# Performance work log

Hardware: AMD Instinct MI355X
Metric: run time of the kernel (lower is better)

Reference implementation:

```python
import jax, jax.numpy as jnp
import numpy as np

N, D, MAX_DEG, B = 100000, 256, 128, 1024
FANOUTS = (25, 10)
OUT = 128  # per-branch output dim; concat doubles it


def setup_inputs() -> dict:
    key = jax.random.key(0)
    ks = jax.random.split(key, 8)
    s1 = 1.0 / np.sqrt(D)
    return {
        "ids": jax.random.randint(ks[0], (B,), 0, N),
        "adj": jax.random.randint(ks[1], (N, MAX_DEG), 0, N),
        "feats": jax.random.normal(ks[2], (N, D), dtype=jnp.float32),
        "W1x": jax.random.normal(ks[3], (OUT, D), dtype=jnp.float32) * s1,
        "b1x": jnp.zeros((OUT,), jnp.float32),
        "W1n": jax.random.normal(ks[4], (OUT, D), dtype=jnp.float32) * s1,
        "b1n": jnp.zeros((OUT,), jnp.float32),
        "W2x": jax.random.normal(ks[5], (OUT, 2 * OUT), dtype=jnp.float32) * s1,
        "b2x": jnp.zeros((OUT,), jnp.float32),
        "W2n": jax.random.normal(ks[6], (OUT, 2 * OUT), dtype=jnp.float32) * s1,
        "b2n": jnp.zeros((OUT,), jnp.float32),
    }


def _sample(adj, ids, n_samples, key):
    # uniform_neib_sampler: one shared random column permutation, take first n
    perm = jax.random.permutation(key, adj.shape[1])
    return adj[ids][:, perm[:n_samples]].reshape(-1)  # flattened neighbor ids


def _agg(x, neibs, Wx, bx, Wn, bn, act):
    # MeanAggregator: concat(fc_x(x), fc_neib(mean over neighbors))
    m = neibs.reshape(x.shape[0], -1, neibs.shape[-1]).mean(axis=1)
    out = jnp.concatenate([x @ Wx.T + bx, m @ Wn.T + bn], axis=-1)
    return act(out) if act is not None else out


def reference(ids, adj, feats, W1x, b1x, W1n, b1n, W2x, b2x, W2n, b2n):
    k1, k2 = jax.random.split(jax.random.key(42))
    ids1 = _sample(adj, ids, FANOUTS[0], k1)      # [B*25]
    ids2 = _sample(adj, ids1, FANOUTS[1], k2)     # [B*25*10]
    h = [feats[ids], feats[ids1], feats[ids2]]    # gathers: the memory-bound core
    # layer 1 (relu) applied to each consecutive (self, neighbor) pair
    h = [_agg(h[k], h[k + 1], W1x, b1x, W1n, b1n, jax.nn.relu) for k in range(2)]
    # layer 2 (no activation)
    h = [_agg(h[0], h[1], W2x, b2x, W2n, b2n, None)]
    return h[0]  # [B, 256]
```

## Files before the change

kernel.cpp:

```cpp
#include <hip/hip_runtime.h>
#include <stdint.h>
#include <stddef.h>
#include <algorithm>


#define D       256
#define D4      64
#define BATCH   1024
#define F1      25
#define F2      10
#define MAXDEG  128
#define OUTD    128
#define SP      264
#define ZP      260

struct Perms { int p1[F1]; int p2[F2]; };

static inline uint32_t rotl32(uint32_t x, int d){ return (x<<d)|(x>>(32-d)); }

static void tf2x32(uint32_t k0, uint32_t k1, uint32_t x0, uint32_t x1,
                   uint32_t* o0, uint32_t* o1){
  uint32_t ks0=k0, ks1=k1, ks2 = k0^k1^0x1BD11BDAu;
  static const int rot[2][4] = {{13,15,26,6},{17,29,16,24}};
  x0 += ks0; x1 += ks1;
  for (int g=0; g<5; ++g){
    const int* r = rot[g&1];
    for (int i=0;i<4;++i){ x0 += x1; x1 = rotl32(x1, r[i]) ^ x0; }
    switch(g){
      case 0: x0 += ks1; x1 += ks2 + 1u; break;
      case 1: x0 += ks2; x1 += ks0 + 2u; break;
      case 2: x0 += ks0; x1 += ks1 + 3u; break;
      case 3: x0 += ks1; x1 += ks2 + 4u; break;
      default:x0 += ks2; x1 += ks0 + 5u; break;
    }
  }
  *o0 = x0; *o1 = x1;
}

static void mkperm(uint32_t ka, uint32_t kb, int n, int* outp){
  uint32_t ska, skb;
  tf2x32(ka, kb, 0u, 1u, &ska, &skb);
  uint32_t bits[MAXDEG];
  int idxs[MAXDEG];
  for (int i=0;i<MAXDEG;++i){
    uint32_t y0,y1; tf2x32(ska,skb, 0u,(uint32_t)i, &y0,&y1);
    bits[i] = y0 ^ y1;
    idxs[i] = i;
  }
  std::stable_sort(idxs, idxs+MAXDEG,
                   [&](int a,int b){ return bits[a] < bits[b]; });
  for (int j=0;j<n;++j) outp[j] = idxs[j];
}

static void compute_perms(Perms& P){
  uint32_t k1a,k1b,k2a,k2b;
  tf2x32(0u,42u, 0u,0u, &k1a,&k1b);
  tf2x32(0u,42u, 0u,1u, &k2a,&k2b);
  mkperm(k1a,k1b, F1, P.p1);
  mkperm(k2a,k2b, F2, P.p2);
}

typedef short s16x8 __attribute__((ext_vector_type(8)));
typedef float f32x4 __attribute__((ext_vector_type(4)));

__device__ __forceinline__ uint16_t f2bf(float f){
  uint32_t u = __float_as_uint(f);
  u += 0x7fffu + ((u >> 16) & 1u);
  return (uint16_t)(u >> 16);
}
__device__ __forceinline__ float bf2f(uint16_t h){
  return __uint_as_float(((uint32_t)h) << 16);
}

__global__ __launch_bounds__(256) void pack_k(
    const float* __restrict__ W1x, const float* __restrict__ W1n,
    const float* __restrict__ W2x, const float* __restrict__ W2n,
    uint16_t* __restrict__ WB, float* __restrict__ W2T){
  int g = blockIdx.x*256 + threadIdx.x;
  if (g < 8192){
    int kt = g >> 10, ct = (g >> 6) & 15, lane = g & 63;
    int n = ct*16 + (lane & 15);
    int k = kt*32 + (lane >> 4)*8;
    const float* src = (n < OUTD) ? (W1x + (size_t)n*D + k)
                                  : (W1n + (size_t)(n-OUTD)*D + k);
    float4 f0 = *(const float4*)src;
    float4 f1 = *(const float4*)(src + 4);
    uint32_t p[4] = {
      (uint32_t)f2bf(f0.x) | ((uint32_t)f2bf(f0.y)<<16),
      (uint32_t)f2bf(f0.z) | ((uint32_t)f2bf(f0.w)<<16),
      (uint32_t)f2bf(f1.x) | ((uint32_t)f2bf(f1.y)<<16),
      (uint32_t)f2bf(f1.z) | ((uint32_t)f2bf(f1.w)<<16) };
    *(uint4*)(WB + (size_t)g*8) = *(uint4*)p;
  } else {
    int idx = g - 8192;
    int k = idx >> 8, o = idx & 255;
    W2T[idx] = (o < OUTD) ? W2x[(size_t)o*D + k]
                          : W2n[(size_t)(o-OUTD)*D + k];
  }
}

__global__ __launch_bounds__(256, 4) void mega6_k(
    const float4* __restrict__ feats4,
    const int* __restrict__ ids, const int* __restrict__ adj,
    const uint16_t* __restrict__ WB, const float* __restrict__ W2T,
    const float* __restrict__ b1x, const float* __restrict__ b1n,
    const float* __restrict__ b2x, const float* __restrict__ b2n,
    float* __restrict__ out, Perms P)
{
  __shared__ uint16_t S[64*SP];
  __shared__ float    M2s[D];
  __shared__ float    Z0s[D];
  __shared__ int      sids[26];
  __shared__ int      nidx[F1*F2];

  const int b    = blockIdx.x;
  const int tid  = threadIdx.x;
  const int lane = tid & 63;
  const int w    = tid >> 6;
  const int ln   = lane & 15;
  const int q    = lane >> 4;
  const int id   = ids[b];
  uint16_t* Z = S;

  if (tid < F1) sids[tid] = adj[(size_t)id*MAXDEG + P.p1[tid]];
  if (tid == F1) sids[F1] = id;
  __syncthreads();
  if (tid < F1*F2){
    int j = tid / F2, u = tid - (tid/F2)*F2;
    nidx[tid] = adj[(size_t)sids[j]*MAXDEG + P.p2[u]];
  }
  __syncthreads();

  float4 va[7];
  #pragma unroll
  for (int l=0;l<7;++l){
    int idx = tid + l*256;
    if (idx < 26*D4)
      va[l] = feats4[(size_t)sids[idx>>6]*D4 + (idx&63)];
  }
  #pragma unroll 2
  for (int t=0;t<7;++t){
    int j = w + 4*t;
    if (j < F1){
      const int* np = &nidx[j*F2];
      float4 s = {0.f,0.f,0.f,0.f};
      #pragma unroll
      for (int u=0;u<F2;++u){
        float4 v = feats4[(size_t)np[u]*D4 + lane];
        s.x+=v.x; s.y+=v.y; s.z+=v.z; s.w+=v.w;
      }
      const float inv = 1.f/F2;
      uint32_t p[2] = {
        (uint32_t)f2bf(s.x*inv) | ((uint32_t)f2bf(s.y*inv)<<16),
        (uint32_t)f2bf(s.z*inv) | ((uint32_t)f2bf(s.w*inv)<<16) };
      *(uint2*)(S + (26+j)*SP + lane*4) = *(uint2*)p;
    }
  }
  #pragma unroll
  for (int l=0;l<7;++l){
    int idx = tid + l*256;
    if (idx < 26*D4){
      int r = idx>>6, c4 = idx&63;
      uint32_t p[2] = { (uint32_t)f2bf(va[l].x) | ((uint32_t)f2bf(va[l].y)<<16),
                        (uint32_t)f2bf(va[l].z) | ((uint32_t)f2bf(va[l].w)<<16) };
      *(uint2*)(S + r*SP + c4*4) = *(uint2*)p;
    }
  }
  __syncthreads();

  {
    float s = 0.f;
    #pragma unroll
    for (int r=0;r<F1;++r) s += bf2f(S[r*SP + tid]);
    S[51*SP + tid] = f2bf(s * (1.f/F1));
  }
  __syncthreads();

  f32x4 acc[4][4];
  #pragma unroll
  for (int mt=0;mt<4;++mt)
    #pragma unroll
    for (int nt=0;nt<4;++nt) acc[mt][nt] = (f32x4){0.f,0.f,0.f,0.f};

  #pragma unroll 2
  for (int kt = 0; kt < 8; ++kt){
    s16x8 af[4], bf[4];
    #pragma unroll
    for (int mt=0;mt<4;++mt)
      af[mt] = *(const s16x8*)(S + (mt*16 + ln)*SP + kt*32 + q*8);
    #pragma unroll
    for (int nt=0;nt<4;++nt)
      bf[nt] = *(const s16x8*)(WB + (size_t)((kt*16 + w*4 + nt)*64 + lane)*8);
    #pragma unroll
    for (int mt=0;mt<4;++mt)
      #pragma unroll
      for (int nt=0;nt<4;++nt)
        acc[mt][nt] = __builtin_amdgcn_mfma_f32_16x16x32_bf16(
                        af[mt], bf[nt], acc[mt][nt], 0, 0, 0);
  }
  __syncthreads();

  {
    const bool left = (w < 2);
    float bia[4];
    #pragma unroll
    for (int nt=0;nt<4;++nt){
      int n = w*64 + nt*16 + ln;
      bia[nt] = left ? b1x[n] : b1n[n-OUTD];
    }
    #pragma unroll
    for (int mt=0;mt<4;++mt)
      #pragma unroll
      for (int nt=0;nt<4;++nt){
        int n = w*64 + nt*16 + ln;
        #pragma unroll
        for (int reg=0;reg<4;++reg){
          int m = mt*16 + q*4 + reg;
          float val = fmaxf(acc[mt][nt][reg] + bia[nt], 0.f);
          if (left){
            if (m < 26) Z[m*ZP + n] = f2bf(val);
            if (m == 25) Z0s[n] = val;
          } else {
            if (m >= 26 && m < 52) Z[(m-26)*ZP + n] = f2bf(val);
            if (m == 51) Z0s[n] = val;
          }
        }
      }
  }
  __syncthreads();

  {
    float s = 0.f;
    #pragma unroll
    for (int r=0;r<F1;++r) s += bf2f(Z[r*ZP + tid]);
    M2s[tid] = s * (1.f/F1);
  }
  __syncthreads();

  {
    const int o = tid;
    const float* zsrc = (o < OUTD) ? Z0s : M2s;
    float acc2 = 0.f;
    #pragma unroll 4
    for (int k4=0;k4<D4;++k4){
      float4 z = *(const float4*)(zsrc + k4*4);
      acc2 += z.x * W2T[(size_t)(k4*4+0)*D + o];
      acc2 += z.y * W2T[(size_t)(k4*4+1)*D + o];
      acc2 += z.z * W2T[(size_t)(k4*4+2)*D + o];
      acc2 += z.w * W2T[(size_t)(k4*4+3)*D + o];
    }
    acc2 += (o < OUTD) ? b2x[o] : b2n[o-OUTD];
    out[(size_t)b*D + o] = acc2;
  }
}

extern "C" void kernel_launch(void* const* d_in, const int* in_sizes, int n_in,
                              void* d_out, int out_size, void* d_ws, size_t ws_size,
                              hipStream_t stream){
  const int*   ids   = (const int*)  d_in[0];
  const int*   adj   = (const int*)  d_in[1];
  const float* feats = (const float*)d_in[2];
  const float* W1x   = (const float*)d_in[3];
  const float* b1x   = (const float*)d_in[4];
  const float* W1n   = (const float*)d_in[5];
  const float* b1n   = (const float*)d_in[6];
  const float* W2x   = (const float*)d_in[7];
  const float* b2x   = (const float*)d_in[8];
  const float* W2n   = (const float*)d_in[9];
  const float* b2n   = (const float*)d_in[10];
  float* out = (float*)d_out;

  Perms P;
  compute_perms(P);

  char* wsb = (char*)d_ws;
  uint16_t* WB  = (uint16_t*)wsb;
  wsb += (size_t)8192*8*sizeof(uint16_t);
  float*    W2T = (float*)wsb;

  hipLaunchKernelGGL(pack_k, dim3(288), dim3(256), 0, stream,
                     W1x, W1n, W2x, W2n, WB, W2T);
  hipLaunchKernelGGL(mega6_k, dim3(BATCH), dim3(256), 0, stream,
                     (const float4*)feats, ids, adj, WB, W2T,
                     b1x, b1n, b2x, b2n, out, P);
}
```

Baseline: 227.3 us.

## Batch neighbor gathers, prefetch all weight fragments early, split layer-2 accumulators

The neighbor-mean loop now issues all ten gathers per row before summing, so more memory requests are in flight, and it is fully unrolled over 6 iterations plus a tail row handled by wave 0. All 32 bf16 weight fragments per wave are loaded into registers before the MFMA phase, hiding global latency behind the self-feature conversion and the syncs. The layer-2 dot product uses four independent accumulators to shorten its dependency chain. Together these raise register pressure a lot (va[7], v[10], bf[8][4], acc[16]) under launch_bounds(256,4), which risks spills or lower occupancy.

```diff
diff --git a/kernel.cpp b/kernel.cpp
--- a/kernel.cpp
+++ b/kernel.cpp
@@ -99,7 +99,7 @@
   }
 }
 
-__global__ __launch_bounds__(256, 4) void mega6_k(
+__global__ __launch_bounds__(256, 4) void mega7_k(
     const float4* __restrict__ feats4,
     const int* __restrict__ ids, const int* __restrict__ adj,
     const uint16_t* __restrict__ WB, const float* __restrict__ W2T,
@@ -138,24 +138,52 @@
     if (idx < 26*D4)
       va[l] = feats4[(size_t)sids[idx>>6]*D4 + (idx&63)];
   }
-  #pragma unroll 2
-  for (int t=0;t<7;++t){
-    int j = w + 4*t;
-    if (j < F1){
-      const int* np = &nidx[j*F2];
-      float4 s = {0.f,0.f,0.f,0.f};
-      #pragma unroll
-      for (int u=0;u<F2;++u){
-        float4 v = feats4[(size_t)np[u]*D4 + lane];
-        s.x+=v.x; s.y+=v.y; s.z+=v.z; s.w+=v.w;
-      }
-      const float inv = 1.f/F2;
-      uint32_t p[2] = {
-        (uint32_t)f2bf(s.x*inv) | ((uint32_t)f2bf(s.y*inv)<<16),
-        (uint32_t)f2bf(s.z*inv) | ((uint32_t)f2bf(s.w*inv)<<16) };
-      *(uint2*)(S + (26+j)*SP + lane*4) = *(uint2*)p;
-    }
-  }
+
+  #pragma unroll
+  for (int t=0;t<6;++t){
+    const int j = w + 4*t;
+    const int* np = &nidx[j*F2];
+    float4 v[F2];
+    #pragma unroll
+    for (int u=0;u<F2;++u)
+      v[u] = feats4[(size_t)np[u]*D4 + lane];
+    float4 s = v[0];
+    #pragma unroll
+    for (int u=1;u<F2;++u){
+      s.x+=v[u].x; s.y+=v[u].y; s.z+=v[u].z; s.w+=v[u].w;
+    }
+    const float inv = 1.f/F2;
+    uint32_t p[2] = {
+      (uint32_t)f2bf(s.x*inv) | ((uint32_t)f2bf(s.y*inv)<<16),
+      (uint32_t)f2bf(s.z*inv) | ((uint32_t)f2bf(s.w*inv)<<16) };
+    *(uint2*)(S + (26+j)*SP + lane*4) = *(uint2*)p;
+  }
+  if (w == 0){
+    const int j = 24;
+    const int* np = &nidx[j*F2];
+    float4 v[F2];
+    #pragma unroll
+    for (int u=0;u<F2;++u)
+      v[u] = feats4[(size_t)np[u]*D4 + lane];
+    float4 s = v[0];
+    #pragma unroll
+    for (int u=1;u<F2;++u){
+      s.x+=v[u].x; s.y+=v[u].y; s.z+=v[u].z; s.w+=v[u].w;
+    }
+    const float inv = 1.f/F2;
+    uint32_t p[2] = {
+      (uint32_t)f2bf(s.x*inv) | ((uint32_t)f2bf(s.y*inv)<<16),
+      (uint32_t)f2bf(s.z*inv) | ((uint32_t)f2bf(s.w*inv)<<16) };
+    *(uint2*)(S + (26+j)*SP + lane*4) = *(uint2*)p;
+  }
+
+  s16x8 bf[8][4];
+  #pragma unroll
+  for (int kt=0;kt<8;++kt)
+    #pragma unroll
+    for (int nt=0;nt<4;++nt)
+      bf[kt][nt] = *(const s16x8*)(WB + (size_t)((kt*16 + w*4 + nt)*64 + lane)*8);
+
   #pragma unroll
   for (int l=0;l<7;++l){
     int idx = tid + l*256;
@@ -182,21 +210,18 @@
     #pragma unroll
     for (int nt=0;nt<4;++nt) acc[mt][nt] = (f32x4){0.f,0.f,0.f,0.f};
 
-  #pragma unroll 2
+  #pragma unroll
   for (int kt = 0; kt < 8; ++kt){
-    s16x8 af[4], bf[4];
+    s16x8 af[4];
     #pragma unroll
     for (int mt=0;mt<4;++mt)
       af[mt] = *(const s16x8*)(S + (mt*16 + ln)*SP + kt*32 + q*8);
-    #pragma unroll
-    for (int nt=0;nt<4;++nt)
-      bf[nt] = *(const s16x8*)(WB + (size_t)((kt*16 + w*4 + nt)*64 + lane)*8);
     #pragma unroll
     for (int mt=0;mt<4;++mt)
       #pragma unroll
       for (int nt=0;nt<4;++nt)
         acc[mt][nt] = __builtin_amdgcn_mfma_f32_16x16x32_bf16(
-                        af[mt], bf[nt], acc[mt][nt], 0, 0, 0);
+                        af[mt], bf[kt][nt], acc[mt][nt], 0, 0, 0);
   }
   __syncthreads();
 
@@ -240,15 +265,17 @@
   {
     const int o = tid;
     const float* zsrc = (o < OUTD) ? Z0s : M2s;
-    float acc2 = 0.f;
-    #pragma unroll 4
+    float a0=0.f, a1=0.f, a2=0.f, a3=0.f;
+    #pragma unroll 8
     for (int k4=0;k4<D4;++k4){
       float4 z = *(const float4*)(zsrc + k4*4);
-      acc2 += z.x * W2T[(size_t)(k4*4+0)*D + o];
-      acc2 += z.y * W2T[(size_t)(k4*4+1)*D + o];
-      acc2 += z.z * W2T[(size_t)(k4*4+2)*D + o];
-      acc2 += z.w * W2T[(size_t)(k4*4+3)*D + o];
-    }
+      const float* wp = W2T + (size_t)k4*4*D + o;
+      a0 += z.x * wp[0];
+      a1 += z.y * wp[D];
+      a2 += z.z * wp[2*D];
+      a3 += z.w * wp[3*D];
+    }
+    float acc2 = (a0 + a2) + (a1 + a3);
     acc2 += (o < OUTD) ? b2x[o] : b2n[o-OUTD];
     out[(size_t)b*D + o] = acc2;
   }
@@ -280,7 +307,7 @@
 
   hipLaunchKernelGGL(pack_k, dim3(288), dim3(256), 0, stream,
                      W1x, W1n, W2x, W2n, WB, W2T);
-  hipLaunchKernelGGL(mega6_k, dim3(BATCH), dim3(256), 0, stream,
+  hipLaunchKernelGGL(mega7_k, dim3(BATCH), dim3(256), 0, stream,
                      (const float4*)feats, ids, adj, WB, W2T,
                      b1x, b1n, b2x, b2n, out, P);
 }
```

Measured after the change: 251.1 us. +10.5%, slower.
